# Kernel tuning notes

Hardware: AMD Instinct MI355X
Metric: run time of the kernel (lower is better)

Reference implementation:

```python
import jax, jax.numpy as jnp
import numpy as np

N = 10000
K = 16
MEAN_NODES = 625.0  # N / K


def setup_inputs() -> dict:
    key = jax.random.key(0)
    k1, k2, k3 = jax.random.split(key, 3)
    # Y: soft partition assignments [N, K]; keep strictly positive so gamma > 0
    Y = jax.random.uniform(k1, (N, K), dtype=jnp.float32, minval=0.01, maxval=1.0)
    # A: dense adjacency / edge-weight matrix [N, N]
    A = jax.random.uniform(k2, (N, N), dtype=jnp.float32)
    # degree: per-node degree column vector [N, 1]
    degree = jax.random.uniform(k3, (N, 1), dtype=jnp.float32, minval=0.5, maxval=2.0)
    return {"Y": Y, "A": A, "degree": degree}


def reference(Y, A, degree):
    # gamma_k = sum_i Y[i,k] * degree[i]  -> [K, 1]
    gamma = Y.T @ degree                      # [K, 1]
    Yn = Y / gamma.reshape(1, K)              # divide column k by gamma_k, [N, K]
    # error_cut = sum_ij A_ij * (Yn @ (1 - Y^T))_ij
    error_cut = ((Yn @ (1.0 - Y.T)) * A).sum()
    # error_partition = sum_k (sum_i Y[i,k] - mean_nodes)^2
    col_sums = Y.sum(axis=0)                  # [K]
    error_partition = jnp.square(col_sums - MEAN_NODES).sum()
    return error_cut + error_partition
```

## Files before the change

kernel.cpp:

```cpp
#include <hip/hip_runtime.h>

#define N_NODES 10000
#define K_COLS 16
#define MEAN_NODES 625.0f

#define WS_PART_OFF 64
#define WS_YT_OFF 4096
#define PREP_BLOCKS 40

__global__ __launch_bounds__(256) void prep_partial(const float* __restrict__ Y,
                                                    const float* __restrict__ deg,
                                                    float* __restrict__ ws) {
    const int b = blockIdx.x;
    const int t = threadIdx.x;
    const int i = b * 250 + t;
    const bool valid = (t < 250);

    float y[K_COLS];
    float d = 0.f;
    if (valid) {
        d = deg[i];
        const float4* yp = (const float4*)(Y + (size_t)i * K_COLS);
        *(float4*)(y + 0)  = yp[0];
        *(float4*)(y + 4)  = yp[1];
        *(float4*)(y + 8)  = yp[2];
        *(float4*)(y + 12) = yp[3];
        float* yt = ws + WS_YT_OFF;
#pragma unroll
        for (int k = 0; k < K_COLS; ++k) yt[(size_t)k * N_NODES + i] = y[k];
    } else {
#pragma unroll
        for (int k = 0; k < K_COLS; ++k) y[k] = 0.f;
    }

    float g[K_COLS], c[K_COLS];
#pragma unroll
    for (int k = 0; k < K_COLS; ++k) { g[k] = y[k] * d; c[k] = y[k]; }

#pragma unroll
    for (int k = 0; k < K_COLS; ++k) {
        for (int off = 32; off > 0; off >>= 1) {
            g[k] += __shfl_down(g[k], off);
            c[k] += __shfl_down(c[k], off);
        }
    }

    __shared__ float red[4][32];
    const int wave = t >> 6, lane = t & 63;
    if (lane == 0) {
#pragma unroll
        for (int k = 0; k < K_COLS; ++k) {
            red[wave][k] = g[k];
            red[wave][K_COLS + k] = c[k];
        }
    }
    __syncthreads();

    if (t < 32) {
        float v = red[0][t] + red[1][t] + red[2][t] + red[3][t];
        ws[WS_PART_OFF + b * 32 + t] = v;
    }
}

__global__ __launch_bounds__(64) void prep_final(float* __restrict__ ws,
                                                 float* __restrict__ out) {
    const int t = threadIdx.x;
    if (t < 32) {
        float v = 0.f;
#pragma unroll
        for (int b = 0; b < PREP_BLOCKS; ++b) v += ws[WS_PART_OFF + b * 32 + t];
        if (t < 16) {
            ws[t] = 1.0f / v;
        } else {
            float dlt = v - MEAN_NODES;
            float sq = dlt * dlt;
            for (int off = 8; off > 0; off >>= 1) sq += __shfl_down(sq, off, 16);
            if (t == 16) out[0] = sq;
        }
    }
}

#define STEPS_PER_SEG 8

__global__ __launch_bounds__(256) void gap_main(const float* __restrict__ A,
                                                const float* __restrict__ Y,
                                                const float* __restrict__ ws,
                                                float* __restrict__ out) {
    const float* __restrict__ YT = ws + WS_YT_OFF;
    const int wave = threadIdx.x >> 6;
    const int lane = threadIdx.x & 63;
    const int rowbase = blockIdx.x * 16 + wave * 4;

    float acc[4][K_COLS];
    float rowsum[4];
#pragma unroll
    for (int r = 0; r < 4; ++r) {
        rowsum[r] = 0.f;
#pragma unroll
        for (int k = 0; k < K_COLS; ++k) acc[r][k] = 0.f;
    }

    const float* __restrict__ Abase = A + (size_t)rowbase * N_NODES;
    const int jstart = (blockIdx.y * STEPS_PER_SEG << 8) + (lane << 2);

    bool v_cur = jstart < N_NODES;
    int jc_cur = v_cur ? jstart : 0;
    float4 a0, a1, a2, a3;
    {
        const float* p = Abase + jc_cur;
        a0 = *(const float4*)(p);
        a1 = *(const float4*)(p + N_NODES);
        a2 = *(const float4*)(p + 2 * (size_t)N_NODES);
        a3 = *(const float4*)(p + 3 * (size_t)N_NODES);
        if (!v_cur) {
            a0 = a1 = a2 = a3 = make_float4(0.f, 0.f, 0.f, 0.f);
        }
    }

#pragma unroll 1
    for (int s = 0; s < STEPS_PER_SEG; ++s) {
        const int jnext = jstart + ((s + 1) << 8);
        const bool v_next = (s + 1 < STEPS_PER_SEG) && (jnext < N_NODES);
        const int jc_next = v_next ? jnext : 0;
        const float* pn = Abase + jc_next;
        float4 b0 = *(const float4*)(pn);
        float4 b1 = *(const float4*)(pn + N_NODES);
        float4 b2 = *(const float4*)(pn + 2 * (size_t)N_NODES);
        float4 b3 = *(const float4*)(pn + 3 * (size_t)N_NODES);
        if (!v_next) {
            b0 = b1 = b2 = b3 = make_float4(0.f, 0.f, 0.f, 0.f);
        }

        rowsum[0] += (a0.x + a0.y) + (a0.z + a0.w);
        rowsum[1] += (a1.x + a1.y) + (a1.z + a1.w);
        rowsum[2] += (a2.x + a2.y) + (a2.z + a2.w);
        rowsum[3] += (a3.x + a3.y) + (a3.z + a3.w);

        const float* ytp = YT + jc_cur;
#pragma unroll
        for (int k = 0; k < K_COLS; ++k) {
            const float4 y = *(const float4*)(ytp + (size_t)k * N_NODES);
            acc[0][k] += a0.x * y.x + a0.y * y.y + a0.z * y.z + a0.w * y.w;
            acc[1][k] += a1.x * y.x + a1.y * y.y + a1.z * y.z + a1.w * y.w;
            acc[2][k] += a2.x * y.x + a2.y * y.y + a2.z * y.z + a2.w * y.w;
            acc[3][k] += a3.x * y.x + a3.y * y.y + a3.z * y.z + a3.w * y.w;
        }

        a0 = b0; a1 = b1; a2 = b2; a3 = b3;
        jc_cur = jc_next;
    }

    __shared__ float rgs[K_COLS];
    if (threadIdx.x < K_COLS) rgs[threadIdx.x] = ws[threadIdx.x];
    __syncthreads();

    float partial = 0.f;
#pragma unroll
    for (int r = 0; r < 4; ++r) {
        const int row = rowbase + r;
        const float* yrow = Y + (size_t)row * K_COLS;
        float s_i = 0.f, dotv = 0.f;
#pragma unroll
        for (int k = 0; k < K_COLS; ++k) {
            const float yn = yrow[k] * rgs[k];
            s_i += yn;
            dotv += yn * acc[r][k];
        }
        partial += s_i * rowsum[r] - dotv;
    }

    for (int off = 32; off > 0; off >>= 1) partial += __shfl_down(partial, off);
    __shared__ float wpart[4];
    if (lane == 0) wpart[wave] = partial;
    __syncthreads();
    if (threadIdx.x == 0)
        atomicAdd(out, (wpart[0] + wpart[1]) + (wpart[2] + wpart[3]));
}

extern "C" void kernel_launch(void* const* d_in, const int* in_sizes, int n_in,
                              void* d_out, int out_size, void* d_ws, size_t ws_size,
                              hipStream_t stream) {
    const float* Y   = (const float*)d_in[0];
    const float* A   = (const float*)d_in[1];
    const float* deg = (const float*)d_in[2];
    float* out = (float*)d_out;
    float* ws  = (float*)d_ws;

    hipLaunchKernelGGL(prep_partial, dim3(PREP_BLOCKS), dim3(256), 0, stream, Y, deg, ws);
    hipLaunchKernelGGL(prep_final, dim3(1), dim3(64), 0, stream, ws, out);
    hipLaunchKernelGGL(gap_main, dim3(N_NODES / 16, 5), dim3(256), 0, stream,
                       A, Y, ws, out);
}
```

Baseline: 564.4 us.

## Reorganize main kernel to tile over row segments with normalized Y in LDS

The main reduction now has each block handle 100 rows and 1024 columns of A. Normalized Y rows and their sums are staged once in shared memory and broadcast, and each thread accumulates column-oriented partials that are dotted with Y[j] at the end. This removes the transposed Y copy written by the prep kernel and the per-step global YT loads, so the loop mostly streams A. The cost is 64+ accumulator registers per thread under a 3-blocks-per-SM launch bound, plus a new grid shape (10x100).

```diff
diff --git a/kernel.cpp b/kernel.cpp
--- a/kernel.cpp
+++ b/kernel.cpp
@@ -5,7 +5,6 @@
 #define MEAN_NODES 625.0f
 
 #define WS_PART_OFF 64
-#define WS_YT_OFF 4096
 #define PREP_BLOCKS 40
 
 __global__ __launch_bounds__(256) void prep_partial(const float* __restrict__ Y,
@@ -25,9 +24,6 @@
         *(float4*)(y + 4)  = yp[1];
         *(float4*)(y + 8)  = yp[2];
         *(float4*)(y + 12) = yp[3];
-        float* yt = ws + WS_YT_OFF;
-#pragma unroll
-        for (int k = 0; k < K_COLS; ++k) yt[(size_t)k * N_NODES + i] = y[k];
     } else {
 #pragma unroll
         for (int k = 0; k < K_COLS; ++k) y[k] = 0.f;
@@ -80,100 +76,104 @@
     }
 }
 
-#define STEPS_PER_SEG 8
+#define ROWS_PER_SEG 100
+#define JT_WIDTH 1024
 
-__global__ __launch_bounds__(256) void gap_main(const float* __restrict__ A,
-                                                const float* __restrict__ Y,
-                                                const float* __restrict__ ws,
-                                                float* __restrict__ out) {
-    const float* __restrict__ YT = ws + WS_YT_OFF;
-    const int wave = threadIdx.x >> 6;
-    const int lane = threadIdx.x & 63;
-    const int rowbase = blockIdx.x * 16 + wave * 4;
+__device__ __forceinline__ void accum_row(const float4 a, const float* __restrict__ ynrow,
+                                          const float si,
+                                          float d[4][K_COLS], float r[4]) {
+    const float av0 = a.x, av1 = a.y, av2 = a.z, av3 = a.w;
+    r[0] += av0 * si; r[1] += av1 * si; r[2] += av2 * si; r[3] += av3 * si;
+    float yn[K_COLS];
+    *(float4*)(yn + 0)  = *(const float4*)(ynrow + 0);
+    *(float4*)(yn + 4)  = *(const float4*)(ynrow + 4);
+    *(float4*)(yn + 8)  = *(const float4*)(ynrow + 8);
+    *(float4*)(yn + 12) = *(const float4*)(ynrow + 12);
+#pragma unroll
+    for (int k = 0; k < K_COLS; ++k) {
+        d[0][k] += av0 * yn[k];
+        d[1][k] += av1 * yn[k];
+        d[2][k] += av2 * yn[k];
+        d[3][k] += av3 * yn[k];
+    }
+}
 
-    float acc[4][K_COLS];
-    float rowsum[4];
+__global__ __launch_bounds__(256, 3) void gap_main(const float* __restrict__ A,
+                                                   const float* __restrict__ Y,
+                                                   const float* __restrict__ ws,
+                                                   float* __restrict__ out) {
+    __shared__ float YnL[ROWS_PER_SEG][K_COLS];
+    __shared__ float sL[ROWS_PER_SEG];
+
+    const int t = threadIdx.x;
+    const int i0 = blockIdx.y * ROWS_PER_SEG;
+    const int j0 = blockIdx.x * JT_WIDTH + (t << 2);
+    const bool jvalid = j0 < N_NODES;
+    const int jc = jvalid ? j0 : (N_NODES - 4);
+
+    if (t < ROWS_PER_SEG) {
+        const float* yrow = Y + (size_t)(i0 + t) * K_COLS;
+        float yn[K_COLS];
+        float s = 0.f;
 #pragma unroll
-    for (int r = 0; r < 4; ++r) {
-        rowsum[r] = 0.f;
+        for (int k = 0; k < K_COLS; ++k) {
+            yn[k] = yrow[k] * ws[k];
+            s += yn[k];
+        }
 #pragma unroll
-        for (int k = 0; k < K_COLS; ++k) acc[r][k] = 0.f;
+        for (int k = 0; k < K_COLS; ++k) YnL[t][k] = yn[k];
+        sL[t] = s;
+    }
+    __syncthreads();
+
+    float d[4][K_COLS];
+    float r[4] = {0.f, 0.f, 0.f, 0.f};
+#pragma unroll
+    for (int jj = 0; jj < 4; ++jj)
+#pragma unroll
+        for (int k = 0; k < K_COLS; ++k) d[jj][k] = 0.f;
+
+    const float* __restrict__ Ab = A + (size_t)i0 * N_NODES + jc;
+
+    float4 a0 = *(const float4*)(Ab);
+    float4 a1 = *(const float4*)(Ab + N_NODES);
+
+#pragma unroll 1
+    for (int ii = 0; ii < ROWS_PER_SEG; ii += 2) {
+        const int n2 = (ii + 2 < ROWS_PER_SEG) ? ii + 2 : ROWS_PER_SEG - 1;
+        const int n3 = (ii + 3 < ROWS_PER_SEG) ? ii + 3 : ROWS_PER_SEG - 1;
+        const float4 p0 = *(const float4*)(Ab + (size_t)n2 * N_NODES);
+        const float4 p1 = *(const float4*)(Ab + (size_t)n3 * N_NODES);
+
+        accum_row(a0, &YnL[ii][0],     sL[ii],     d, r);
+        accum_row(a1, &YnL[ii + 1][0], sL[ii + 1], d, r);
+
+        a0 = p0; a1 = p1;
     }
 
-    const float* __restrict__ Abase = A + (size_t)rowbase * N_NODES;
-    const int jstart = (blockIdx.y * STEPS_PER_SEG << 8) + (lane << 2);
-
-    bool v_cur = jstart < N_NODES;
-    int jc_cur = v_cur ? jstart : 0;
-    float4 a0, a1, a2, a3;
-    {
-        const float* p = Abase + jc_cur;
-        a0 = *(const float4*)(p);
-        a1 = *(const float4*)(p + N_NODES);
-        a2 = *(const float4*)(p + 2 * (size_t)N_NODES);
-        a3 = *(const float4*)(p + 3 * (size_t)N_NODES);
-        if (!v_cur) {
-            a0 = a1 = a2 = a3 = make_float4(0.f, 0.f, 0.f, 0.f);
+    float partial = 0.f;
+    if (jvalid) {
+#pragma unroll
+        for (int jj = 0; jj < 4; ++jj) {
+            const float* yj = Y + (size_t)(j0 + jj) * K_COLS;
+            float yv[K_COLS];
+            *(float4*)(yv + 0)  = *(const float4*)(yj + 0);
+            *(float4*)(yv + 4)  = *(const float4*)(yj + 4);
+            *(float4*)(yv + 8)  = *(const float4*)(yj + 8);
+            *(float4*)(yv + 12) = *(const float4*)(yj + 12);
+            float dot = 0.f;
+#pragma unroll
+            for (int k = 0; k < K_COLS; ++k) dot += d[jj][k] * yv[k];
+            partial += r[jj] - dot;
         }
-    }
-
-#pragma unroll 1
-    for (int s = 0; s < STEPS_PER_SEG; ++s) {
-        const int jnext = jstart + ((s + 1) << 8);
-        const bool v_next = (s + 1 < STEPS_PER_SEG) && (jnext < N_NODES);
-        const int jc_next = v_next ? jnext : 0;
-        const float* pn = Abase + jc_next;
-        float4 b0 = *(const float4*)(pn);
-        float4 b1 = *(const float4*)(pn + N_NODES);
-        float4 b2 = *(const float4*)(pn + 2 * (size_t)N_NODES);
-        float4 b3 = *(const float4*)(pn + 3 * (size_t)N_NODES);
-        if (!v_next) {
-            b0 = b1 = b2 = b3 = make_float4(0.f, 0.f, 0.f, 0.f);
-        }
-
-        rowsum[0] += (a0.x + a0.y) + (a0.z + a0.w);
-        rowsum[1] += (a1.x + a1.y) + (a1.z + a1.w);
-        rowsum[2] += (a2.x + a2.y) + (a2.z + a2.w);
-        rowsum[3] += (a3.x + a3.y) + (a3.z + a3.w);
-
-        const float* ytp = YT + jc_cur;
-#pragma unroll
-        for (int k = 0; k < K_COLS; ++k) {
-            const float4 y = *(const float4*)(ytp + (size_t)k * N_NODES);
-            acc[0][k] += a0.x * y.x + a0.y * y.y + a0.z * y.z + a0.w * y.w;
-            acc[1][k] += a1.x * y.x + a1.y * y.y + a1.z * y.z + a1.w * y.w;
-            acc[2][k] += a2.x * y.x + a2.y * y.y + a2.z * y.z + a2.w * y.w;
-            acc[3][k] += a3.x * y.x + a3.y * y.y + a3.z * y.z + a3.w * y.w;
-        }
-
-        a0 = b0; a1 = b1; a2 = b2; a3 = b3;
-        jc_cur = jc_next;
-    }
-
-    __shared__ float rgs[K_COLS];
-    if (threadIdx.x < K_COLS) rgs[threadIdx.x] = ws[threadIdx.x];
-    __syncthreads();
-
-    float partial = 0.f;
-#pragma unroll
-    for (int r = 0; r < 4; ++r) {
-        const int row = rowbase + r;
-        const float* yrow = Y + (size_t)row * K_COLS;
-        float s_i = 0.f, dotv = 0.f;
-#pragma unroll
-        for (int k = 0; k < K_COLS; ++k) {
-            const float yn = yrow[k] * rgs[k];
-            s_i += yn;
-            dotv += yn * acc[r][k];
-        }
-        partial += s_i * rowsum[r] - dotv;
     }
 
     for (int off = 32; off > 0; off >>= 1) partial += __shfl_down(partial, off);
     __shared__ float wpart[4];
+    const int wave = t >> 6, lane = t & 63;
     if (lane == 0) wpart[wave] = partial;
     __syncthreads();
-    if (threadIdx.x == 0)
+    if (t == 0)
         atomicAdd(out, (wpart[0] + wpart[1]) + (wpart[2] + wpart[3]));
 }
 
@@ -188,6 +188,5 @@
 
     hipLaunchKernelGGL(prep_partial, dim3(PREP_BLOCKS), dim3(256), 0, stream, Y, deg, ws);
     hipLaunchKernelGGL(prep_final, dim3(1), dim3(64), 0, stream, ws, out);
-    hipLaunchKernelGGL(gap_main, dim3(N_NODES / 16, 5), dim3(256), 0, stream,
-                       A, Y, ws, out);
+    hipLaunchKernelGGL(gap_main, dim3(10, 100), dim3(256), 0, stream, A, Y, ws, out);
 }
```

Result: faster. 538.4 us (-4.6%).
